# Performance work log

Measured on AMD Instinct MI355X. Metric: run time of the kernel, lower is better.

Reference implementation:

```python
import jax, jax.numpy as jnp
import numpy as np
from jax import lax

NPOINT = 1024
K = 32
EPS = 1e-5  # BatchNorm2d default eps


def setup_inputs() -> dict:
    key = jax.random.key(0)
    ks = jax.random.split(key, 8)
    B, N = 16, 4096
    xyz = jax.random.normal(ks[0], (B, N, 3), dtype=jnp.float32)
    init_farthest = jax.random.randint(ks[1], (B,), 0, N, dtype=jnp.int32)
    def w(k, o, i):
        return jax.random.normal(k, (o, i), dtype=jnp.float32) * (1.0 / np.sqrt(i))
    chans = [3, 64, 64, 128]
    inp = {"xyz": xyz, "init_farthest": init_farthest}
    for li in range(3):
        ci, co = chans[li], chans[li + 1]
        inp[f"W{li+1}"] = w(ks[2 + li], co, ci)
        inp[f"b{li+1}"] = jnp.zeros((co,), jnp.float32)
        inp[f"g{li+1}"] = jnp.ones((co,), jnp.float32)
        inp[f"be{li+1}"] = jnp.zeros((co,), jnp.float32)
    return inp


def _farthest_point_sample(xyz, init_farthest, npoint):
    # Sequential FPS: npoint iterations of distance-update + argmax (lax.scan).
    B, N, _ = xyz.shape
    bidx = jnp.arange(B)
    def step(carry, _):
        distance, farthest = carry
        centroid = xyz[bidx, farthest][:, None, :]            # [B,1,3]
        d = jnp.sum((xyz - centroid) ** 2, axis=-1)           # [B,N]
        distance = jnp.minimum(distance, d)
        return (distance, jnp.argmax(distance, axis=-1)), farthest
    init = (jnp.full((B, N), 1e10, xyz.dtype), init_farthest)
    _, centroids = lax.scan(step, init, None, length=npoint)  # [npoint,B]
    return centroids.T                                        # [B,npoint]


def _forward(xyz, init_farthest, params):
    B, N, _ = xyz.shape
    fps_idx = _farthest_point_sample(xyz, init_farthest, NPOINT)      # [B,S]
    bidx = jnp.arange(B)[:, None]
    new_xyz = xyz[bidx, fps_idx]                                       # [B,S,3]
    # KNN over sampled points (pairwise squared distances, [B,S,S])
    dist = jnp.sum((new_xyz[:, :, None, :] - new_xyz[:, None, :, :]) ** 2, axis=-1)
    idx = jnp.argsort(dist, axis=-1)[:, :, 1:K + 1]                    # [B,S,K]
    # NOTE: faithful to original code: idx (values < npoint) indexes xyz rows.
    grouped = xyz[jnp.arange(B)[:, None, None], idx]                   # [B,S,K,3]
    grouped = grouped - new_xyz[:, :, None, :]
    x = jnp.transpose(grouped, (0, 3, 1, 2))                           # [B,3,S,K]
    for (W, b, g, be) in params:
        x = jnp.einsum('oc,bcsk->bosk', W, x) + b[None, :, None, None]
        m = x.mean(axis=(0, 2, 3), keepdims=True)
        v = x.var(axis=(0, 2, 3), keepdims=True)                       # biased var (BN train mode)
        x = g[None, :, None, None] * (x - m) * lax.rsqrt(v + EPS) + be[None, :, None, None]
        x = jax.nn.relu(x)
    new_points = jnp.max(x, axis=-1)                                   # [B,128,S]
    return new_xyz, new_points


def reference(xyz, init_farthest, W1, b1, g1, be1, W2, b2, g2, be2, W3, b3, g3, be3):
    params = [(W1, b1, g1, be1), (W2, b2, g2, be2), (W3, b3, g3, be3)]
    return _forward(xyz, init_farthest, params)
```

## Files before the change

kernel.cpp:

```cpp
#include <hip/hip_runtime.h>


#define Bc 16
#define Nn 4096
#define Ss 1024
#define Kk 32
#define COLS (Bc*Ss*Kk)
#define EPSF 1e-5f

typedef unsigned long long ull;
typedef unsigned int uint32;

__device__ __forceinline__ unsigned short f2bf(float f){
  uint32 u = __float_as_uint(f);
  uint32 r = (u + 0x7fffu + ((u>>16)&1u)) >> 16;
  return (unsigned short)r;
}
__device__ __forceinline__ float bf2f(unsigned short h){ return __uint_as_float(((uint32)h)<<16); }

__device__ __forceinline__ float dppmax_f32(float x){
  #define STEPF(ctrl,rm) { int _s=__builtin_amdgcn_update_dpp(__float_as_int(x),__float_as_int(x),(ctrl),(rm),0xf,false); x=fmaxf(x,__int_as_float(_s)); }
  STEPF(0x111,0xf) STEPF(0x112,0xf) STEPF(0x114,0xf) STEPF(0x118,0xf)
  STEPF(0x142,0xa) STEPF(0x143,0xc)
  #undef STEPF
  return __int_as_float(__builtin_amdgcn_readlane(__float_as_int(x),63));
}
__device__ __forceinline__ int dppmin_i32(int x){
  #define STEPI(ctrl,rm) { int _s=__builtin_amdgcn_update_dpp(x,x,(ctrl),(rm),0xf,false); x=min(x,_s); }
  STEPI(0x111,0xf) STEPI(0x112,0xf) STEPI(0x114,0xf) STEPI(0x118,0xf)
  STEPI(0x142,0xa) STEPI(0x143,0xc)
  #undef STEPI
  return __builtin_amdgcn_readlane(x,63);
}

__global__ __launch_bounds__(256) void fps_kernel(const float* __restrict__ xyz,
                                                  const int* __restrict__ init_far,
                                                  float* __restrict__ new_xyz){
  __shared__ float sx[Nn*3];
  __shared__ ull wk[2][4];
  int b = blockIdx.x, t = threadIdx.x;
  int lane = t & 63, wid = t >> 6;
  const float4* xb4 = (const float4*)(xyz + (size_t)b*Nn*3);
  float4* sx4 = (float4*)sx;
  for(int i=t;i<Nn*3/4;i+=256) sx4[i]=xb4[i];
  __syncthreads();
  float px[16],py[16],pz[16],dd[16];
  #pragma unroll
  for(int j=0;j<16;j++){ int n=t+256*j; px[j]=sx[n*3]; py[j]=sx[n*3+1]; pz[j]=sx[n*3+2]; dd[j]=1e10f; }
  int far = init_far[b];
  float o0x=0.f,o0y=0.f,o0z=0.f, o1x=0.f,o1y=0.f,o1z=0.f;
  float o2x=0.f,o2y=0.f,o2z=0.f, o3x=0.f,o3y=0.f,o3z=0.f;
  for(int it=0; it<Ss; it++){
    float cx=sx[far*3], cy=sx[far*3+1], cz=sx[far*3+2];
    if(t==(it&255)){
      if(it<256)      { o0x=cx; o0y=cy; o0z=cz; }
      else if(it<512) { o1x=cx; o1y=cy; o1z=cz; }
      else if(it<768) { o2x=cx; o2y=cy; o2z=cz; }
      else            { o3x=cx; o3y=cy; o3z=cz; }
    }
    #pragma unroll
    for(int j=0;j<16;j++){
      float dx=px[j]-cx, dy=py[j]-cy, dz=pz[j]-cz;
      float d=__fadd_rn(__fadd_rn(__fmul_rn(dx,dx),__fmul_rn(dy,dy)),__fmul_rn(dz,dz));
      dd[j]=fminf(dd[j],d);
    }
    float m0=fmaxf(fmaxf(fmaxf(dd[0],dd[1]),fmaxf(dd[2],dd[3])),fmaxf(fmaxf(dd[4],dd[5]),fmaxf(dd[6],dd[7])));
    float m1=fmaxf(fmaxf(fmaxf(dd[8],dd[9]),fmaxf(dd[10],dd[11])),fmaxf(fmaxf(dd[12],dd[13]),fmaxf(dd[14],dd[15])));
    float bd=fmaxf(m0,m1);
    float dmax = dppmax_f32(bd);
    int cj=16;
    #pragma unroll
    for(int j=15;j>=0;j--) cj = (dd[j]!=dmax) ? cj : j;
    int cand = t + (cj<<8);
    int wmin = dppmin_i32(cand);
    if(lane==0) wk[it&1][wid] = ((ull)__float_as_uint(dmax)<<32) | (uint32)(4095-wmin);
    __syncthreads();
    ull g0=wk[it&1][0], g1=wk[it&1][1], g2=wk[it&1][2], g3=wk[it&1][3];
    ull ka = g1>g0?g1:g0, kb = g3>g2?g3:g2;
    ull kg = kb>ka?kb:ka;
    far = 4095-(int)(uint32)(kg&0xffffffffu);
  }
  float* outb = new_xyz + (size_t)b*Ss*3;
  outb[t*3+0]=o0x; outb[t*3+1]=o0y; outb[t*3+2]=o0z;
  outb[(256+t)*3+0]=o1x; outb[(256+t)*3+1]=o1y; outb[(256+t)*3+2]=o1z;
  outb[(512+t)*3+0]=o2x; outb[(512+t)*3+1]=o2y; outb[(512+t)*3+2]=o2z;
  outb[(768+t)*3+0]=o3x; outb[(768+t)*3+1]=o3y; outb[(768+t)*3+2]=o3z;
}

#define KN16(X) X(0) X(1) X(2) X(3) X(4) X(5) X(6) X(7) X(8) X(9) X(10) X(11) X(12) X(13) X(14) X(15)

__global__ __launch_bounds__(256) void knn_kernel(const float* __restrict__ xyz,
                                                  const float* __restrict__ new_xyz,
                                                  float* __restrict__ gout){
  __shared__ float nx[Ss*3];
  int b = blockIdx.x >> 8;
  int t = threadIdx.x;
  const float4* src=(const float4*)(new_xyz + (size_t)b*Ss*3);
  float4* dst=(float4*)nx;
  for(int i=t;i<Ss*3/4;i+=256) dst[i]=src[i];
  __syncthreads();
  int wid=t>>6, lane=t&63;
  int s=(blockIdx.x&255)*4+wid;
  float qx=nx[s*3],qy=nx[s*3+1],qz=nx[s*3+2];
  #define KDECL(i) ull K##i;
  KN16(KDECL)
  #undef KDECL
  #define KINIT(i) { int j=lane+64*(i); \
    float dx=nx[j*3]-qx, dy=nx[j*3+1]-qy, dz=nx[j*3+2]-qz; \
    float d=__fadd_rn(__fadd_rn(__fmul_rn(dx,dx),__fmul_rn(dy,dy)),__fmul_rn(dz,dz)); \
    K##i=((ull)(__float_as_uint(d)+1u)<<32)|(uint32)(j); }
  KN16(KINIT)
  #undef KINIT
  ull last=0; int myn=0;
  for(int r=0;r<33;r++){
    ull cur=~0ull;
    #define KSCAN(i) { ull c=K##i; c=(c>last)?c:~0ull; cur=(c<cur)?c:cur; }
    KN16(KSCAN)
    #undef KSCAN
    #pragma unroll
    for(int m=32;m>=1;m>>=1){ ull o=__shfl_xor(cur,m,64); cur = o<cur?o:cur; }
    last=cur;
    if(r>=1 && lane==r-1) myn=(int)(uint32)(cur&0xffffffffu);
  }
  if(lane<Kk){
    int j=myn;
    const float* p=xyz + (size_t)b*Nn*3 + (size_t)j*3;
    float* go = gout + ((size_t)(b*Ss+s)*Kk + lane)*3;
    go[0]=p[0]-qx; go[1]=p[1]-qy; go[2]=p[2]-qz;
  }
}

__global__ __launch_bounds__(256) void gmom_kernel(const float* __restrict__ g, float* __restrict__ stats){
  __shared__ float sm[9];
  int t=threadIdx.x;
  if(t<9) sm[t]=0.f;
  __syncthreads();
  float a[9]={0,0,0,0,0,0,0,0,0};
  for(int col=blockIdx.x*256+t; col<COLS; col+=gridDim.x*256){
    float x=g[(size_t)col*3],y=g[(size_t)col*3+1],z=g[(size_t)col*3+2];
    a[0]+=x;a[1]+=y;a[2]+=z;a[3]+=x*x;a[4]+=y*y;a[5]+=z*z;a[6]+=x*y;a[7]+=x*z;a[8]+=y*z;
  }
  #pragma unroll
  for(int i=0;i<9;i++){
    float v=a[i];
    #pragma unroll
    for(int m=32;m>=1;m>>=1) v+=__shfl_xor(v,m,64);
    if((t&63)==0) atomicAdd(&sm[i],v);
  }
  __syncthreads();
  if(t<9) atomicAdd(&stats[t],sm[t]);
}

__global__ __launch_bounds__(256) void layer12_kernel(const float* __restrict__ g,
    const float* __restrict__ W1,const float* __restrict__ b1,const float* __restrict__ g1,const float* __restrict__ be1,
    const float* __restrict__ W2,const float* __restrict__ b2,
    const float* __restrict__ stats, unsigned short* __restrict__ y2){
  __shared__ float x2s[64*128];
  __shared__ float w2s[64*65];
  __shared__ float w1s[192], b1s[64], sc1[64], sh1[64], b2s[64];
  int t=threadIdx.x;
  for(int i=t;i<4096;i+=256){ w2s[(i>>6)*65+(i&63)]=W2[i]; }
  if(t<192) w1s[t]=W1[t];
  if(t<64){ b1s[t]=b1[t]; b2s[t]=b2[t]; }
  __syncthreads();
  if(t<64){
    const float n1=1.0f/COLS;
    float ex=stats[0]*n1,ey=stats[1]*n1,ez=stats[2]*n1;
    float cxx=stats[3]*n1-ex*ex, cyy=stats[4]*n1-ey*ey, czz=stats[5]*n1-ez*ez;
    float cxy=stats[6]*n1-ex*ey, cxz=stats[7]*n1-ex*ez, cyz=stats[8]*n1-ey*ez;
    float wx=w1s[t*3],wy=w1s[t*3+1],wz=w1s[t*3+2];
    float m=wx*ex+wy*ey+wz*ez+b1s[t];
    float v=wx*wx*cxx+wy*wy*cyy+wz*wz*czz+2.f*(wx*wy*cxy+wx*wz*cxz+wy*wz*cyz);
    float sc=g1[t]*rsqrtf(v+EPSF);
    sc1[t]=sc; sh1[t]=be1[t]-m*sc;
  }
  __syncthreads();
  {
    int col=t&127, c0=(t>>7)*32;
    size_t cg=(size_t)blockIdx.x*128+col;
    float gx=g[cg*3],gy=g[cg*3+1],gz=g[cg*3+2];
    for(int c=c0;c<c0+32;c++){
      float y=fmaf(w1s[c*3],gx,fmaf(w1s[c*3+1],gy,fmaf(w1s[c*3+2],gz,b1s[c])));
      x2s[c*128+col]=fmaxf(fmaf(y,sc1[c],sh1[c]),0.f);
    }
  }
  __syncthreads();
  int og=t>>4, cgi=t&15;
  float acc[4][8];
  #pragma unroll
  for(int r=0;r<4;r++){ float bb=b2s[og*4+r];
    #pragma unroll
    for(int j=0;j<8;j++) acc[r][j]=bb; }
  for(int c=0;c<64;c++){
    float xv[8];
    #pragma unroll
    for(int j=0;j<8;j++) xv[j]=x2s[c*128+cgi+16*j];
    #pragma unroll
    for(int r=0;r<4;r++){
      float w=w2s[(og*4+r)*65+c];
      #pragma unroll
      for(int j=0;j<8;j++) acc[r][j]=fmaf(w,xv[j],acc[r][j]);
    }
  }
  #pragma unroll
  for(int j=0;j<8;j++){
    size_t col=(size_t)blockIdx.x*128+cgi+16*j;
    ushort4 pk;
    pk.x=f2bf(acc[0][j]); pk.y=f2bf(acc[1][j]); pk.z=f2bf(acc[2][j]); pk.w=f2bf(acc[3][j]);
    *(ushort4*)(y2 + col*64 + og*4)=pk;
  }
}

__global__ __launch_bounds__(256) void stats2_kernel(const unsigned short* __restrict__ y2, float* __restrict__ stats){
  __shared__ float red[128];
  int t=threadIdx.x;
  if(t<128) red[t]=0.f;
  __syncthreads();
  int c4=t&15;
  float s[4]={0,0,0,0}, q[4]={0,0,0,0};
  int col=(blockIdx.x*256+t)>>4;
  int stride=(gridDim.x*256)>>4;
  for(; col<COLS; col+=stride){
    ushort4 u=*(const ushort4*)(y2+(size_t)col*64+c4*4);
    float f0=bf2f(u.x),f1=bf2f(u.y),f2=bf2f(u.z),f3=bf2f(u.w);
    s[0]+=f0;s[1]+=f1;s[2]+=f2;s[3]+=f3;
    q[0]=fmaf(f0,f0,q[0]);q[1]=fmaf(f1,f1,q[1]);q[2]=fmaf(f2,f2,q[2]);q[3]=fmaf(f3,f3,q[3]);
  }
  #pragma unroll
  for(int e=0;e<4;e++){ atomicAdd(&red[c4*4+e],s[e]); atomicAdd(&red[64+c4*4+e],q[e]); }
  __syncthreads();
  if(t<64) atomicAdd(&stats[16+t],red[t]);
  else if(t<128) atomicAdd(&stats[80+(t-64)],red[t]);
}

__global__ __launch_bounds__(256) void layer3_kernel(const unsigned short* __restrict__ y2,
    const float* __restrict__ g2,const float* __restrict__ be2,
    const float* __restrict__ W3,const float* __restrict__ b3,
    float* __restrict__ stats, float* __restrict__ ymax, float* __restrict__ ymin){
  __shared__ float x3s[64*64];
  __shared__ unsigned short w3s[128*66];
  __shared__ float y3s[128*65];
  __shared__ float sc2[64], sh2[64], b3s[128];
  int t=threadIdx.x;
  if(t<64){
    const float n1=1.0f/COLS;
    float m=stats[16+t]*n1;
    float v=stats[80+t]*n1-m*m;
    float sc=g2[t]*rsqrtf(v+EPSF);
    sc2[t]=sc; sh2[t]=be2[t]-m*sc;
  }
  if(t<128) b3s[t]=b3[t];
  for(int i=t;i<8192;i+=256){ w3s[(i>>6)*66+(i&63)]=f2bf(W3[i]); }
  __syncthreads();
  int og=t>>4, cgi=t&15;
  int q=t>>7, oo=t&127;
  float asum=0.f, asq=0.f;
  const uint32* w3u=(const uint32*)w3s;
  for(int tl=0; tl<4; tl++){
    int colbase=(blockIdx.x*4+tl)*64;
    {
      int col=t&63, c0=(t>>6)*16;
      const unsigned short* yp=y2+(size_t)(colbase+col)*64+c0;
      #pragma unroll
      for(int h=0;h<2;h++){
        uint4 u=((const uint4*)yp)[h];
        uint32 ua[4]={u.x,u.y,u.z,u.w};
        #pragma unroll
        for(int e=0;e<4;e++){
          int c=c0+h*8+e*2;
          float flo=__uint_as_float(ua[e]<<16);
          float fhi=__uint_as_float(ua[e]&0xffff0000u);
          x3s[c*64+col]=fmaxf(fmaf(flo,sc2[c],sh2[c]),0.f);
          x3s[(c+1)*64+col]=fmaxf(fmaf(fhi,sc2[c+1],sh2[c+1]),0.f);
        }
      }
    }
    __syncthreads();
    float acc[8][4];
    #pragma unroll
    for(int r=0;r<8;r++){ float bb=b3s[og*8+r];
      #pragma unroll
      for(int j=0;j<4;j++) acc[r][j]=bb; }
    for(int c2=0;c2<32;c2++){
      float x0[4],x1[4];
      #pragma unroll
      for(int j=0;j<4;j++){ x0[j]=x3s[(2*c2)*64+cgi+16*j]; x1[j]=x3s[(2*c2+1)*64+cgi+16*j]; }
      #pragma unroll
      for(int r=0;r<8;r++){
        uint32 w=w3u[(og*8+r)*33+c2];
        float w0=__uint_as_float(w<<16);
        float w1=__uint_as_float(w&0xffff0000u);
        #pragma unroll
        for(int j=0;j<4;j++) acc[r][j]=fmaf(w1,x1[j],fmaf(w0,x0[j],acc[r][j]));
      }
    }
    #pragma unroll
    for(int r=0;r<8;r++){
      #pragma unroll
      for(int j=0;j<4;j++) y3s[(og*8+r)*65+cgi+16*j]=acc[r][j];
    }
    __syncthreads();
    {
      float mx=-3.4e38f, mn=3.4e38f, su=0.f, sq=0.f;
      #pragma unroll
      for(int k=0;k<32;k++){
        float yv=y3s[oo*65+q*32+k];
        mx=fmaxf(mx,yv); mn=fminf(mn,yv); su+=yv; sq=fmaf(yv,yv,sq);
      }
      asum+=su; asq+=sq;
      int qg=(colbase>>5)+q;
      int bb=qg>>10, ss=qg&1023;
      ymax[((size_t)bb*128+oo)*1024+ss]=mx;
      ymin[((size_t)bb*128+oo)*1024+ss]=mn;
    }
    __syncthreads();
  }
  if(t>=128){ x3s[t-128]=asum; x3s[128+(t-128)]=asq; }
  __syncthreads();
  if(t<128){
    asum+=x3s[t]; asq+=x3s[128+t];
    atomicAdd(&stats[144+t],asum);
    atomicAdd(&stats[272+t],asq);
  }
}

__global__ __launch_bounds__(256) void finalize_kernel(const float* __restrict__ ymax,const float* __restrict__ ymin,
    const float* __restrict__ g3,const float* __restrict__ be3,const float* __restrict__ stats,
    float* __restrict__ outp){
  int idx=blockIdx.x*256+threadIdx.x;
  int o=(idx>>10)&127;
  const float n1=1.0f/COLS;
  float m=stats[144+o]*n1;
  float v=stats[272+o]*n1-m*m;
  float sc=g3[o]*rsqrtf(v+EPSF);
  float sh=be3[o]-m*sc;
  float val=(sc>=0.f)?ymax[idx]:ymin[idx];
  outp[idx]=fmaxf(fmaf(val,sc,sh),0.f);
}

extern "C" void kernel_launch(void* const* d_in, const int* in_sizes, int n_in,
                              void* d_out, int out_size, void* d_ws, size_t ws_size,
                              hipStream_t stream){
  const float* xyz=(const float*)d_in[0];
  const int* initf=(const int*)d_in[1];
  const float* W1=(const float*)d_in[2]; const float* b1=(const float*)d_in[3];
  const float* g1=(const float*)d_in[4]; const float* be1=(const float*)d_in[5];
  const float* W2=(const float*)d_in[6]; const float* b2=(const float*)d_in[7];
  const float* g2=(const float*)d_in[8]; const float* be2=(const float*)d_in[9];
  const float* W3=(const float*)d_in[10]; const float* b3=(const float*)d_in[11];
  const float* g3=(const float*)d_in[12]; const float* be3=(const float*)d_in[13];
  float* out=(float*)d_out;
  char* ws=(char*)d_ws;
  float* gbuf=(float*)(ws+65536);
  float* stats=(float*)(ws+6356992);
  unsigned short* y2=(unsigned short*)(ws+6361088);
  float* ymax=(float*)(ws+73469952);
  float* ymin=(float*)(ws+81858560);
  hipMemsetAsync(stats,0,4096,stream);
  fps_kernel<<<16,256,0,stream>>>(xyz,initf,out);
  knn_kernel<<<4096,256,0,stream>>>(xyz,out,gbuf);
  gmom_kernel<<<1024,256,0,stream>>>(gbuf,stats);
  layer12_kernel<<<4096,256,0,stream>>>(gbuf,W1,b1,g1,be1,W2,b2,stats,y2);
  stats2_kernel<<<2048,256,0,stream>>>(y2,stats);
  layer3_kernel<<<2048,256,0,stream>>>(y2,g2,be2,W3,b3,stats,ymax,ymin);
  finalize_kernel<<<8192,256,0,stream>>>(ymax,ymin,g3,be3,stats,out+49152);
}
```

Baseline: 1.197 ms.

## Pad FPS points to float4, DPP min in KNN, fuse layer-2 stats, replicate atomics

FPS now stores points in shared memory as padded float4, so the centroid and per-thread points are read with single vector loads. The KNN selection replaces 64-bit shuffle reductions with two 32-bit DPP min reductions, first on distance and then on index. The separate stats2 pass over y2 is removed: layer-2 sums and sums of squares are accumulated inside layer12 from the fp32 accumulators. BN2 and BN3 stats atomics are spread across 8 replicas to cut contention, at the cost of a larger memset. Taking layer-2 stats before bf16 rounding slightly changes the numerics.

```diff
diff --git a/kernel.cpp b/kernel.cpp
--- a/kernel.cpp
+++ b/kernel.cpp
@@ -8,6 +8,11 @@
 #define COLS (Bc*Ss*Kk)
 #define EPSF 1e-5f
 
+#define S2SUM 16
+#define S2SQ  528
+#define S3SUM 1040
+#define S3SQ  2064
+
 typedef unsigned long long ull;
 typedef unsigned int uint32;
 
@@ -36,22 +41,31 @@
 __global__ __launch_bounds__(256) void fps_kernel(const float* __restrict__ xyz,
                                                   const int* __restrict__ init_far,
                                                   float* __restrict__ new_xyz){
-  __shared__ float sx[Nn*3];
+  __shared__ float sx[Nn*4];
   __shared__ ull wk[2][4];
   int b = blockIdx.x, t = threadIdx.x;
   int lane = t & 63, wid = t >> 6;
-  const float4* xb4 = (const float4*)(xyz + (size_t)b*Nn*3);
-  float4* sx4 = (float4*)sx;
-  for(int i=t;i<Nn*3/4;i+=256) sx4[i]=xb4[i];
-  __syncthreads();
+  const float* xb = xyz + (size_t)b*Nn*3;
+  const float4* xb4 = (const float4*)xb;
+  for(int i=t;i<Nn*3/4;i+=256){
+    float4 v = xb4[i];
+    int f0 = 4*i;
+    sx[(f0/3)*4 + (f0%3)]       = v.x;
+    sx[((f0+1)/3)*4 + ((f0+1)%3)] = v.y;
+    sx[((f0+2)/3)*4 + ((f0+2)%3)] = v.z;
+    sx[((f0+3)/3)*4 + ((f0+3)%3)] = v.w;
+  }
+  __syncthreads();
+  const float4* sxp = (const float4*)sx;
   float px[16],py[16],pz[16],dd[16];
   #pragma unroll
-  for(int j=0;j<16;j++){ int n=t+256*j; px[j]=sx[n*3]; py[j]=sx[n*3+1]; pz[j]=sx[n*3+2]; dd[j]=1e10f; }
+  for(int j=0;j<16;j++){ int n=t+256*j; float4 p=sxp[n]; px[j]=p.x; py[j]=p.y; pz[j]=p.z; dd[j]=1e10f; }
   int far = init_far[b];
   float o0x=0.f,o0y=0.f,o0z=0.f, o1x=0.f,o1y=0.f,o1z=0.f;
   float o2x=0.f,o2y=0.f,o2z=0.f, o3x=0.f,o3y=0.f,o3z=0.f;
   for(int it=0; it<Ss; it++){
-    float cx=sx[far*3], cy=sx[far*3+1], cz=sx[far*3+2];
+    float4 c4 = sxp[far];
+    float cx=c4.x, cy=c4.y, cz=c4.z;
     if(t==(it&255)){
       if(it<256)      { o0x=cx; o0y=cy; o0z=cz; }
       else if(it<512) { o1x=cx; o1y=cy; o1z=cz; }
@@ -117,10 +131,13 @@
     #define KSCAN(i) { ull c=K##i; c=(c>last)?c:~0ull; cur=(c<cur)?c:cur; }
     KN16(KSCAN)
     #undef KSCAN
-    #pragma unroll
-    for(int m=32;m>=1;m>>=1){ ull o=__shfl_xor(cur,m,64); cur = o<cur?o:cur; }
-    last=cur;
-    if(r>=1 && lane==r-1) myn=(int)(uint32)(cur&0xffffffffu);
+    int hs=(int)(uint32)(cur>>32);
+    hs = (hs<0) ? 0x7fffffff : hs;
+    int dmin = dppmin_i32(hs);
+    int ci = (hs==dmin) ? (int)(uint32)cur : 0x7fffffff;
+    int jmin = dppmin_i32(ci);
+    last = ((ull)(uint32)dmin<<32)|(uint32)jmin;
+    if(r>=1 && lane==r-1) myn=jmin;
   }
   if(lane<Kk){
     int j=myn;
@@ -154,14 +171,16 @@
 __global__ __launch_bounds__(256) void layer12_kernel(const float* __restrict__ g,
     const float* __restrict__ W1,const float* __restrict__ b1,const float* __restrict__ g1,const float* __restrict__ be1,
     const float* __restrict__ W2,const float* __restrict__ b2,
-    const float* __restrict__ stats, unsigned short* __restrict__ y2){
+    const float* __restrict__ stats, unsigned short* __restrict__ y2,
+    float* __restrict__ statsw){
   __shared__ float x2s[64*128];
   __shared__ float w2s[64*65];
   __shared__ float w1s[192], b1s[64], sc1[64], sh1[64], b2s[64];
+  __shared__ float rs2[64], rq2[64];
   int t=threadIdx.x;
   for(int i=t;i<4096;i+=256){ w2s[(i>>6)*65+(i&63)]=W2[i]; }
   if(t<192) w1s[t]=W1[t];
-  if(t<64){ b1s[t]=b1[t]; b2s[t]=b2[t]; }
+  if(t<64){ b1s[t]=b1[t]; b2s[t]=b2[t]; rs2[t]=0.f; rq2[t]=0.f; }
   __syncthreads();
   if(t<64){
     const float n1=1.0f/COLS;
@@ -209,28 +228,20 @@
     pk.x=f2bf(acc[0][j]); pk.y=f2bf(acc[1][j]); pk.z=f2bf(acc[2][j]); pk.w=f2bf(acc[3][j]);
     *(ushort4*)(y2 + col*64 + og*4)=pk;
   }
-}
-
-__global__ __launch_bounds__(256) void stats2_kernel(const unsigned short* __restrict__ y2, float* __restrict__ stats){
-  __shared__ float red[128];
-  int t=threadIdx.x;
-  if(t<128) red[t]=0.f;
-  __syncthreads();
-  int c4=t&15;
-  float s[4]={0,0,0,0}, q[4]={0,0,0,0};
-  int col=(blockIdx.x*256+t)>>4;
-  int stride=(gridDim.x*256)>>4;
-  for(; col<COLS; col+=stride){
-    ushort4 u=*(const ushort4*)(y2+(size_t)col*64+c4*4);
-    float f0=bf2f(u.x),f1=bf2f(u.y),f2=bf2f(u.z),f3=bf2f(u.w);
-    s[0]+=f0;s[1]+=f1;s[2]+=f2;s[3]+=f3;
-    q[0]=fmaf(f0,f0,q[0]);q[1]=fmaf(f1,f1,q[1]);q[2]=fmaf(f2,f2,q[2]);q[3]=fmaf(f3,f3,q[3]);
-  }
-  #pragma unroll
-  for(int e=0;e<4;e++){ atomicAdd(&red[c4*4+e],s[e]); atomicAdd(&red[64+c4*4+e],q[e]); }
-  __syncthreads();
-  if(t<64) atomicAdd(&stats[16+t],red[t]);
-  else if(t<128) atomicAdd(&stats[80+(t-64)],red[t]);
+  #pragma unroll
+  for(int r=0;r<4;r++){
+    float s_=0.f, q_=0.f;
+    #pragma unroll
+    for(int j=0;j<8;j++){ float v=acc[r][j]; s_+=v; q_=fmaf(v,v,q_); }
+    atomicAdd(&rs2[og*4+r],s_);
+    atomicAdd(&rq2[og*4+r],q_);
+  }
+  __syncthreads();
+  if(t<64){
+    int rep=blockIdx.x&7;
+    atomicAdd(&statsw[S2SUM+rep*64+t],rs2[t]);
+    atomicAdd(&statsw[S2SQ +rep*64+t],rq2[t]);
+  }
 }
 
 __global__ __launch_bounds__(256) void layer3_kernel(const unsigned short* __restrict__ y2,
@@ -244,8 +255,11 @@
   int t=threadIdx.x;
   if(t<64){
     const float n1=1.0f/COLS;
-    float m=stats[16+t]*n1;
-    float v=stats[80+t]*n1-m*m;
+    float ssum=0.f, ssq=0.f;
+    #pragma unroll
+    for(int rp=0;rp<8;rp++){ ssum+=stats[S2SUM+rp*64+t]; ssq+=stats[S2SQ+rp*64+t]; }
+    float m=ssum*n1;
+    float v=ssq*n1-m*m;
     float sc=g2[t]*rsqrtf(v+EPSF);
     sc2[t]=sc; sh2[t]=be2[t]-m*sc;
   }
@@ -319,8 +333,9 @@
   __syncthreads();
   if(t<128){
     asum+=x3s[t]; asq+=x3s[128+t];
-    atomicAdd(&stats[144+t],asum);
-    atomicAdd(&stats[272+t],asq);
+    int rep=blockIdx.x&7;
+    atomicAdd(&stats[S3SUM+rep*128+t],asum);
+    atomicAdd(&stats[S3SQ +rep*128+t],asq);
   }
 }
 
@@ -330,8 +345,11 @@
   int idx=blockIdx.x*256+threadIdx.x;
   int o=(idx>>10)&127;
   const float n1=1.0f/COLS;
-  float m=stats[144+o]*n1;
-  float v=stats[272+o]*n1-m*m;
+  float ssum=0.f, ssq=0.f;
+  #pragma unroll
+  for(int rp=0;rp<8;rp++){ ssum+=stats[S3SUM+rp*128+o]; ssq+=stats[S3SQ+rp*128+o]; }
+  float m=ssum*n1;
+  float v=ssq*n1-m*m;
   float sc=g3[o]*rsqrtf(v+EPSF);
   float sh=be3[o]-m*sc;
   float val=(sc>=0.f)?ymax[idx]:ymin[idx];
@@ -351,17 +369,16 @@
   const float* g3=(const float*)d_in[12]; const float* be3=(const float*)d_in[13];
   float* out=(float*)d_out;
   char* ws=(char*)d_ws;
+  float* stats=(float*)(ws);
   float* gbuf=(float*)(ws+65536);
-  float* stats=(float*)(ws+6356992);
   unsigned short* y2=(unsigned short*)(ws+6361088);
   float* ymax=(float*)(ws+73469952);
   float* ymin=(float*)(ws+81858560);
-  hipMemsetAsync(stats,0,4096,stream);
+  hipMemsetAsync(stats,0,16384,stream);
   fps_kernel<<<16,256,0,stream>>>(xyz,initf,out);
   knn_kernel<<<4096,256,0,stream>>>(xyz,out,gbuf);
   gmom_kernel<<<1024,256,0,stream>>>(gbuf,stats);
-  layer12_kernel<<<4096,256,0,stream>>>(gbuf,W1,b1,g1,be1,W2,b2,stats,y2);
-  stats2_kernel<<<2048,256,0,stream>>>(y2,stats);
+  layer12_kernel<<<4096,256,0,stream>>>(gbuf,W1,b1,g1,be1,W2,b2,stats,y2,stats);
   layer3_kernel<<<2048,256,0,stream>>>(y2,g2,be2,W3,b3,stats,ymax,ymin);
   finalize_kernel<<<8192,256,0,stream>>>(ymax,ymin,g3,be3,stats,out+49152);
 }
```

Result: faster. 1.167 ms (-2.6%).
